# Kernel tuning notes

Measured on AMD Instinct MI355X. Metric: run time of the kernel, lower is better.

Reference implementation:

```python
import jax, jax.numpy as jnp
import numpy as np

N_HEADS = 8
EPS = 1e-5  # torch nn.LayerNorm default


def layer_norm(x, g, b):
    mu = jnp.mean(x, axis=-1, keepdims=True)
    var = jnp.var(x, axis=-1, keepdims=True)
    return (x - mu) * jax.lax.rsqrt(var + EPS) * g + b


def mha(q_in, k_in, v_in, adj, Wq, bq, Wk, bk, Wv, bv, Wo, bo, g, be):
    # Standard GL-GIN / Co-guiding MultiHeadAttention: proj -> adjacency-masked
    # scaled dot-product softmax -> out proj -> residual + LayerNorm.
    # Dropout omitted (eval mode).
    B, Lq, D = q_in.shape
    Lk = k_in.shape[1]
    d_k = Wq.shape[-1] // N_HEADS
    q = (q_in @ Wq + bq).reshape(B, Lq, N_HEADS, d_k)
    k = (k_in @ Wk + bk).reshape(B, Lk, N_HEADS, d_k)
    v = (v_in @ Wv + bv).reshape(B, Lk, N_HEADS, d_k)
    scale = jnp.asarray(1.0 / np.sqrt(d_k), q_in.dtype)
    scores = jnp.einsum('bqhd,bkhd->bhqk', q, k) * scale  # [B,H,Lq,Lk]
    neg = jnp.asarray(-1e9, scores.dtype)
    scores = jnp.where(adj[:, None, :, :] == 0, neg, scores)
    attn = jax.nn.softmax(scores, axis=-1)
    out = jnp.einsum('bhqk,bkhd->bqhd', attn, v).reshape(B, Lq, N_HEADS * d_k)
    out = out @ Wo + bo
    return layer_norm(out + q_in, g, be)


def co_guiding_forward(h_a, h_b, adj_a, adj_b, adj_ab, adj_ba,
                       Wq, bq, Wk, bk, Wv, bv, Wo, bo, ln_g, ln_b):
    # Param arrays are stacked [n_layer, 4, ...], branch order: a2a, b2b, a2b, b2a.
    input_a, input_b = h_a, h_b
    n_layer = Wq.shape[0]
    for i in range(n_layer):
        def P(j):
            return (Wq[i, j], bq[i, j], Wk[i, j], bk[i, j], Wv[i, j], bv[i, j],
                    Wo[i, j], bo[i, j], ln_g[i, j], ln_b[i, j])
        a2a = mha(h_a, h_a, h_a, adj_a, *P(0))
        b2b = mha(h_b, h_b, h_b, adj_b, *P(1))
        a2b = mha(h_b, h_a, h_a, adj_ab, *P(2))
        b2a = mha(h_a, h_b, h_b, adj_ba, *P(3))
        h_a = jax.nn.relu(a2a + b2a)
        h_b = jax.nn.relu(b2b + a2b)
    return input_a + h_a, input_b + h_b


def setup_inputs():
    key = jax.random.key(0)
    ks = jax.random.split(key, 16)
    B, N, D, L = 4, 1024, 256, 2
    f = lambda k, s: jax.random.normal(k, s, dtype=jnp.float32) * 0.05
    return {
        'h_a': jax.random.normal(ks[0], (B, N, D), dtype=jnp.float32),
        'h_b': jax.random.normal(ks[1], (B, N, D), dtype=jnp.float32),
        'adj_a': jax.random.randint(ks[2], (B, N, N), 0, 2, dtype=jnp.int32),
        'adj_b': jax.random.randint(ks[3], (B, N, N), 0, 2, dtype=jnp.int32),
        'adj_ab': jax.random.randint(ks[4], (B, N, N), 0, 2, dtype=jnp.int32),
        'adj_ba': jax.random.randint(ks[5], (B, N, N), 0, 2, dtype=jnp.int32),
        'Wq': f(ks[6], (L, 4, D, D)), 'bq': f(ks[7], (L, 4, D)),
        'Wk': f(ks[8], (L, 4, D, D)), 'bk': f(ks[9], (L, 4, D)),
        'Wv': f(ks[10], (L, 4, D, D)), 'bv': f(ks[11], (L, 4, D)),
        'Wo': f(ks[12], (L, 4, D, D)), 'bo': f(ks[13], (L, 4, D)),
        'ln_g': jnp.ones((L, 4, D), dtype=jnp.float32),
        'ln_b': jnp.zeros((L, 4, D), dtype=jnp.float32),
    }


def reference(h_a, h_b, adj_a, adj_b, adj_ab, adj_ba,
              Wq, bq, Wk, bk, Wv, bv, Wo, bo, ln_g, ln_b):
    return co_guiding_forward(h_a, h_b, adj_a, adj_b, adj_ab, adj_ba,
                              Wq, bq, Wk, bk, Wv, bv, Wo, bo, ln_g, ln_b)
```

## Files before the change

kernel.cpp:

```cpp
#include <hip/hip_runtime.h>
#include <hip/hip_bf16.h>
#include <stdint.h>


using bf16x8 = __attribute__((ext_vector_type(8))) short;
using f32x4  = __attribute__((ext_vector_type(4))) float;
using f32x16 = __attribute__((ext_vector_type(16))) float;

#define DEVI __device__ __forceinline__

DEVI uint16_t f2bf(float x) {
  uint32_t u = __float_as_uint(x);
  u += 0x7FFFu + ((u >> 16) & 1u);
  return (uint16_t)(u >> 16);
}
DEVI uint32_t packbf2(float lo, float hi) {
  uint32_t r;
  asm("v_cvt_pk_bf16_f32 %0, %1, %2" : "=v"(r) : "v"(lo), "v"(hi));
  return r;
}
DEVI float bf2f(uint16_t v) { return __uint_as_float((uint32_t)v << 16); }
DEVI int phi4(int m) {
  return ((m & 4) << 1) | ((m & 8) >> 1) | (m & 3);
}

struct PrepArgs {
  const float* Wq; const float* Wk; const float* Wv; const float* Wo;
  uint16_t* wt;
  const float* ha; const float* hb;
  uint16_t* oa; uint16_t* ob;
  const int* adj[4];
  uint32_t* bits[4];
};

__global__ __launch_bounds__(256) void prep_k(PrepArgs a) {
  const int blk = blockIdx.x;
  const int t = threadIdx.x;
  __shared__ float tl[64][68];

  if (blk < 512) {
    const int bx = blk & 3, by = (blk >> 2) & 3, z = blk >> 4;
    const int type = z >> 3, mat = z & 7;
    const float* W = (type == 0 ? a.Wq : type == 1 ? a.Wk : type == 2 ? a.Wv : a.Wo)
                     + (size_t)mat * 65536;
    uint16_t* o = a.wt + (size_t)type * 524288 + (size_t)mat * 65536;
    const int r0 = by * 64, c0 = bx * 64;
    {
      const int rr = t >> 2, cb = (t & 3) * 16;
      const float* src = W + (size_t)(r0 + rr) * 256 + c0 + cb;
      #pragma unroll
      for (int q = 0; q < 4; ++q) {
        float4 v = *(const float4*)(src + q * 4);
        tl[rr][cb + q*4 + 0] = v.x; tl[rr][cb + q*4 + 1] = v.y;
        tl[rr][cb + q*4 + 2] = v.z; tl[rr][cb + q*4 + 3] = v.w;
      }
    }
    __syncthreads();
    {
      const int nn = t >> 2, kb = (t & 3) * 16;
      __align__(16) uint16_t tmp[16];
      #pragma unroll
      for (int q = 0; q < 16; ++q) tmp[q] = f2bf(tl[kb + q][nn]);
      uint16_t* dst = o + (size_t)(c0 + nn) * 256 + r0 + kb;
      *(uint4*)&dst[0] = *(uint4*)&tmp[0];
      *(uint4*)&dst[8] = *(uint4*)&tmp[8];
    }
  } else if (blk < 1536) {
    const int idx = blk - 512;
    const int bx = idx & 511, by = idx >> 9;
    const size_t i = ((size_t)bx * 256 + t) * 8;
    const float* s = by ? a.hb : a.ha;
    uint16_t* o = by ? a.ob : a.oa;
    const float4 f0 = *(const float4*)(s + i), f1 = *(const float4*)(s + i + 4);
    uint4 u;
    u.x = packbf2(f0.x, f0.y); u.y = packbf2(f0.z, f0.w);
    u.z = packbf2(f1.x, f1.y); u.w = packbf2(f1.z, f1.w);
    *(uint4*)(o + i) = u;
  } else {
    const int idx = blk - 1536;
    const int bx = idx & 16383, z = idx >> 14;
    const int* adj = a.adj[z];
    uint32_t* bits = a.bits[z];
    const size_t i = (size_t)bx * 256 + t;
    const int lane = t & 63;
    const int v = adj[i];
    unsigned long long m = __ballot(v != 0);
    if ((lane & 31) == 0) {
      const uint32_t wi = (uint32_t)(i >> 5);
      const uint32_t kw = wi & 31;
      const uint32_t q  = (wi >> 5) & 1023;
      const uint32_t bb = wi >> 15;
      bits[((bb * 32 + kw) << 10) | q] = (uint32_t)(m >> (lane & 32));
    }
  }
}

struct GemmArgs {
  const uint16_t* A[12];
  const uint16_t* W[12];
  const float*    bias[12];
  void*           C[12];
  float           os[12];
  int             mode[12];
};

DEVI void stage_tile(const uint16_t* __restrict__ Ab,
                     const uint16_t* __restrict__ Wt,
                     int m0, int n0, int kk,
                     char* AsB, char* BsB, int wid, int lane) {
  #pragma unroll
  for (int i = 0; i < 2; ++i) {
    const int seg = i * 4 + wid;
    const int rl  = (seg << 4) + (lane >> 2);
    const int gs  = (lane & 3) ^ ((lane >> 3) & 3);
    const uint16_t* gA = Ab + (size_t)(m0 + rl) * 256 + kk + gs * 8;
    const uint16_t* gB = Wt + (size_t)(n0 + rl) * 256 + kk + gs * 8;
    __builtin_amdgcn_global_load_lds(
        (const __attribute__((address_space(1))) void*)gA,
        (__attribute__((address_space(3))) void*)(AsB + (seg << 10)), 16, 0, 0);
    __builtin_amdgcn_global_load_lds(
        (const __attribute__((address_space(1))) void*)gB,
        (__attribute__((address_space(3))) void*)(BsB + (seg << 10)), 16, 0, 0);
  }
}

__global__ __launch_bounds__(256) void gemm_k(GemmArgs args) {
  const int z  = blockIdx.z;
  const int m0 = blockIdx.y * 128, n0 = blockIdx.x * 128;
  const uint16_t* Ab = args.A[z];
  const uint16_t* Wt = args.W[z];
  __shared__ __align__(16) uint16_t As[2][4096];
  __shared__ __align__(16) uint16_t Bs[2][4096];
  const int t = threadIdx.x;
  const int lane = t & 63, wid = t >> 6;
  const int g = lane >> 4, c = lane & 15;
  const int gx = g ^ ((c >> 1) & 3);
  const int wm = (wid >> 1) * 64, wn = (wid & 1) * 64;
  f32x4 acc[4][4] = {};

  stage_tile(Ab, Wt, m0, n0, 0, (char*)As[0], (char*)Bs[0], wid, lane);
  __syncthreads();

  for (int ks = 0; ks < 8; ++ks) {
    const int buf = ks & 1;
    if (ks < 7)
      stage_tile(Ab, Wt, m0, n0, (ks + 1) * 32,
                 (char*)As[buf ^ 1], (char*)Bs[buf ^ 1], wid, lane);
    bf16x8 af[4], bfr[4];
    #pragma unroll
    for (int mt = 0; mt < 4; ++mt)
      af[mt]  = *(const bf16x8*)&As[buf][(wm + mt * 16 + c) * 32 + gx * 8];
    #pragma unroll
    for (int nt = 0; nt < 4; ++nt)
      bfr[nt] = *(const bf16x8*)&Bs[buf][(wn + nt * 16 + c) * 32 + gx * 8];
    #pragma unroll
    for (int mt = 0; mt < 4; ++mt)
      #pragma unroll
      for (int nt = 0; nt < 4; ++nt)
        acc[mt][nt] = __builtin_amdgcn_mfma_f32_16x16x32_bf16(af[mt], bfr[nt], acc[mt][nt], 0, 0, 0);
    if (ks < 7) __syncthreads();
  }

  const float* bias = args.bias[z];
  const float osz = args.os[z];
  const int mode = args.mode[z];
  float bv[4];
  #pragma unroll
  for (int nt = 0; nt < 4; ++nt) bv[nt] = bias[n0 + wn + nt * 16 + c];

  if (mode == 2) {
    uint16_t* C = (uint16_t*)args.C[z];
    __syncthreads();
    uint16_t* ep = ((uint16_t*)As) + wid * (16 * 72);
    #pragma unroll
    for (int mt = 0; mt < 4; ++mt) {
      #pragma unroll
      for (int r = 0; r < 4; ++r)
        #pragma unroll
        for (int nt = 0; nt < 4; ++nt)
          ep[(4 * g + r) * 72 + nt * 16 + c] = f2bf((acc[mt][nt][r] + bv[nt]) * osz);
      #pragma unroll
      for (int sr = 0; sr < 2; ++sr) {
        const int row  = sr * 8 + (lane >> 3);
        const int col8 = (lane & 7) * 8;
        const uint4 v4 = *(const uint4*)&ep[row * 72 + col8];
        const int n  = m0 + wm + mt * 16 + row;
        const int bb = n >> 10, nn = n & 1023;
        const int colg = n0 + wn + col8;
        const int hh = colg >> 5, d = colg & 31;
        *(uint4*)&C[((size_t)(bb * 8 + hh) * 1024 + nn) * 32 + d] = v4;
      }
    }
  } else {
    uint16_t* C = (uint16_t*)args.C[z];
    __syncthreads();
    uint16_t* ep = ((uint16_t*)As) + wid * (64 * 24);
    const int colg = n0 + wn + lane;
    const int hh = colg >> 5, d = colg & 31;
    #pragma unroll
    for (int mt = 0; mt < 4; ++mt) {
      #pragma unroll
      for (int r = 0; r < 4; ++r) {
        const int pn = phi4(4 * g + r);
        #pragma unroll
        for (int nt = 0; nt < 4; ++nt)
          ep[(nt * 16 + c) * 24 + pn] = f2bf((acc[mt][nt][r] + bv[nt]) * osz);
      }
      const int nbase = m0 + wm + mt * 16;
      const int bb = nbase >> 10, nb = nbase & 1023;
      uint16_t* dst = C + ((size_t)(bb * 8 + hh) * 32 + d) * 1024 + nb;
      *(uint4*)dst       = *(const uint4*)&ep[lane * 24];
      *(uint4*)(dst + 8) = *(const uint4*)&ep[lane * 24 + 8];
    }
  }
}

struct AttnArgs {
  const uint16_t* Q[4];
  const uint16_t* K[4];
  const uint16_t* Vt[4];
  const uint32_t* adjb[4];
  uint16_t*       O[4];
};

DEVI void soft_pv(f32x16& st, uint32_t w, float& l,
                  const bf16x8& vf0, const bf16x8& vf1, f32x16& oacc) {
  float s0 = 0.f, s1 = 0.f, s2 = 0.f, s3 = 0.f;
  #pragma unroll
  for (int r = 0; r < 16; ++r) {
    const int pos = (r & 3) + 8 * (r >> 2);
    const uint32_t msk = (uint32_t)__builtin_amdgcn_sbfe((int)w, pos, 1);
    const float pv = __uint_as_float(
        __float_as_uint(__builtin_amdgcn_exp2f(st[r])) & msk);
    st[r] = pv;
    if ((r & 3) == 0) s0 += pv; else if ((r & 3) == 1) s1 += pv;
    else if ((r & 3) == 2) s2 += pv; else s3 += pv;
  }
  l += (s0 + s1) + (s2 + s3);

  union PU { uint32_t u[4]; bf16x8 v; };
  PU p0, p1;
  p0.u[0] = packbf2(st[0],  st[1]);  p0.u[1] = packbf2(st[2],  st[3]);
  p0.u[2] = packbf2(st[4],  st[5]);  p0.u[3] = packbf2(st[6],  st[7]);
  p1.u[0] = packbf2(st[8],  st[9]);  p1.u[1] = packbf2(st[10], st[11]);
  p1.u[2] = packbf2(st[12], st[13]); p1.u[3] = packbf2(st[14], st[15]);

  oacc = __builtin_amdgcn_mfma_f32_32x32x16_bf16(vf0, p0.v, oacc, 0, 0, 0);
  oacc = __builtin_amdgcn_mfma_f32_32x32x16_bf16(vf1, p1.v, oacc, 0, 0, 0);
}

__global__ __launch_bounds__(256) void attn_k(AttnArgs args) {
  const int bid = blockIdx.x;
  const int qt  = bid >> 7;
  const int grp = bid & 127;
  const int bh = grp & 31, j = grp >> 5;
  const int b = bh >> 3, h = bh & 7;
  const int t = threadIdx.x, wid = t >> 6, lane = t & 63;
  const int qg = wid & 1, ks = wid >> 1;
  const int c = lane & 31, hi = lane >> 5;
  const int hsh = hi * 4;
  const int qrow = qt * 128 + qg * 64 + c;

  const uint16_t* Qbh = args.Q[j] + (size_t)(b * 8 + h) * 32768;
  const uint16_t* Kbh = args.K[j] + (size_t)(b * 8 + h) * 32768;
  const uint16_t* Vbh = args.Vt[j] + ((size_t)(b * 8 + h) * 32 + c) * 1024 + hi * 8;

  const bf16x8 qa0 = *(const bf16x8*)&Qbh[qrow * 32 + hi * 8];
  const bf16x8 qa1 = *(const bf16x8*)&Qbh[qrow * 32 + 16 + hi * 8];
  const bf16x8 qb0 = *(const bf16x8*)&Qbh[(qrow + 32) * 32 + hi * 8];
  const bf16x8 qb1 = *(const bf16x8*)&Qbh[(qrow + 32) * 32 + 16 + hi * 8];

  f32x16 oA = {}, oB = {};
  float lA = 0.f, lB = 0.f;

  const int kbeg = ks * 512;
  const uint16_t* kp = Kbh + (size_t)(kbeg + c) * 32 + hi * 8;
  const uint16_t* vp = Vbh + kbeg;
  const uint32_t* ap = args.adjb[j] + (size_t)b * 32768
                       + ((size_t)(kbeg >> 5) << 10) + qrow;

  for (int it = 0; it < 16; ++it) {
    const uint32_t wA = ap[0]  >> hsh;
    const uint32_t wB = ap[32] >> hsh;
    const bf16x8 kf0 = *(const bf16x8*)kp;
    const bf16x8 kf1 = *(const bf16x8*)(kp + 16);
    const bf16x8 vf0 = *(const bf16x8*)vp;
    const bf16x8 vf1 = *(const bf16x8*)(vp + 16);
    ap += 1024; kp += 1024; vp += 32;

    f32x16 sA = {}, sB = {};
    sA = __builtin_amdgcn_mfma_f32_32x32x16_bf16(kf0, qa0, sA, 0, 0, 0);
    sA = __builtin_amdgcn_mfma_f32_32x32x16_bf16(kf1, qa1, sA, 0, 0, 0);
    sB = __builtin_amdgcn_mfma_f32_32x32x16_bf16(kf0, qb0, sB, 0, 0, 0);
    sB = __builtin_amdgcn_mfma_f32_32x32x16_bf16(kf1, qb1, sB, 0, 0, 0);

    soft_pv(sA, wA, lA, vf0, vf1, oA);
    soft_pv(sB, wB, lB, vf0, vf1, oB);
  }

  __shared__ float red[2][2][64][17];
  if (ks == 1) {
    #pragma unroll
    for (int r = 0; r < 16; ++r) {
      red[qg][0][lane][r] = oA[r];
      red[qg][1][lane][r] = oB[r];
    }
    red[qg][0][lane][16] = lA;
    red[qg][1][lane][16] = lB;
  }
  __syncthreads();
  if (ks == 1) return;

  {
    #pragma unroll
    for (int r = 0; r < 16; ++r) {
      oA[r] += red[qg][0][lane][r];
      oB[r] += red[qg][1][lane][r];
    }
    lA += red[qg][0][lane][16];
    lB += red[qg][1][lane][16];
  }

  lA += __shfl_xor(lA, 32, 64);
  lB += __shfl_xor(lB, 32, 64);
  const float invA = 1.0f / lA;
  const float invB = 1.0f / lB;
  uint16_t* O = args.O[j];
  const size_t obA = (size_t)(b * 1024 + qrow) * 256 + h * 32 + 4 * hi;
  const size_t obB = obA + (size_t)32 * 256;
  #pragma unroll
  for (int rq = 0; rq < 4; ++rq) {
    uint2 vA, vB;
    vA.x = packbf2(oA[4*rq+0] * invA, oA[4*rq+1] * invA);
    vA.y = packbf2(oA[4*rq+2] * invA, oA[4*rq+3] * invA);
    vB.x = packbf2(oB[4*rq+0] * invB, oB[4*rq+1] * invB);
    vB.y = packbf2(oB[4*rq+2] * invB, oB[4*rq+3] * invB);
    *(uint2*)&O[obA + 8 * rq] = vA;
    *(uint2*)&O[obB + 8 * rq] = vB;
  }
}

struct OplnArgs {
  const uint16_t* A0[2]; const uint16_t* A1[2];
  const uint16_t* W0[2]; const uint16_t* W1[2];
  const float*    b0[2]; const float*    b1[2];
  const uint16_t* res[2];
  const float* g0[2]; const float* be0[2];
  const float* g1[2]; const float* be1[2];
  const float* addin[2];
  float*     outf[2];
  uint16_t*  outbf[2];
};

__global__ __launch_bounds__(256) void opln_k(OplnArgs args) {
  const int side = blockIdx.y;
  const int m0 = blockIdx.x * 32;
  const uint16_t* A0 = args.A0[side];
  const uint16_t* A1 = args.A1[side];
  const uint16_t* W0 = args.W0[side];
  const uint16_t* W1 = args.W1[side];

  __shared__ __align__(16) char lds[76800];
  uint16_t* As0 = (uint16_t*)(lds);
  uint16_t* As1 = (uint16_t*)(lds + 4096);
  uint16_t* Bs0 = (uint16_t*)(lds + 8192);
  uint16_t* Bs1 = (uint16_t*)(lds + 8192 + 32768);
  float*    red = (float*)(lds + 8192 + 65536);
  float*    muv = (float*)(lds + 8192 + 65536 + 2048);
  uint16_t* outt = (uint16_t*)lds;

  const int t = threadIdx.x;
  const int lane = t & 63, wid = t >> 6;
  const int g = lane >> 4, c = lane & 15;
  const int gx = g ^ ((c >> 1) & 3);
  const int gs = (lane & 3) ^ ((lane >> 3) & 3);

  auto stage = [&](int buf, int kk) {
    {
      const uint16_t* src = (wid < 2) ? A0 : A1;
      char* dst = (char*)((wid < 2) ? As0 : As1) + (size_t)buf * 2048 + ((wid & 1) << 10);
      const int rl = ((wid & 1) << 4) + (lane >> 2);
      __builtin_amdgcn_global_load_lds(
          (const __attribute__((address_space(1))) void*)(src + (size_t)(m0 + rl) * 256 + kk + gs * 8),
          (__attribute__((address_space(3))) void*)dst, 16, 0, 0);
    }
    #pragma unroll
    for (int i = 0; i < 8; ++i) {
      const int s32 = i * 4 + wid;
      const int mat = s32 >> 4, seg = s32 & 15;
      const uint16_t* src = mat ? W1 : W0;
      char* dst = (char*)(mat ? Bs1 : Bs0) + (size_t)buf * 16384 + (seg << 10);
      const int rl = (seg << 4) + (lane >> 2);
      __builtin_amdgcn_global_load_lds(
          (const __attribute__((address_space(1))) void*)(src + (size_t)rl * 256 + kk + gs * 8),
          (__attribute__((address_space(3))) void*)dst, 16, 0, 0);
    }
  };

  f32x4 a0[2][4] = {}, a1[2][4] = {};
  stage(0, 0);
  __syncthreads();

  for (int ks = 0; ks < 8; ++ks) {
    const int buf = ks & 1;
    if (ks < 7) stage(buf ^ 1, (ks + 1) * 32);
    const uint16_t* As0b = As0 + buf * 1024;
    const uint16_t* As1b = As1 + buf * 1024;
    const uint16_t* Bs0b = Bs0 + buf * 8192;
    const uint16_t* Bs1b = Bs1 + buf * 8192;
    bf16x8 fa0[2], fa1[2], fb0[4], fb1[4];
    #pragma unroll
    for (int mt = 0; mt < 2; ++mt) {
      fa0[mt] = *(const bf16x8*)&As0b[(mt * 16 + c) * 32 + gx * 8];
      fa1[mt] = *(const bf16x8*)&As1b[(mt * 16 + c) * 32 + gx * 8];
    }
    #pragma unroll
    for (int nt = 0; nt < 4; ++nt) {
      fb0[nt] = *(const bf16x8*)&Bs0b[(wid * 64 + nt * 16 + c) * 32 + gx * 8];
      fb1[nt] = *(const bf16x8*)&Bs1b[(wid * 64 + nt * 16 + c) * 32 + gx * 8];
    }
    #pragma unroll
    for (int mt = 0; mt < 2; ++mt)
      #pragma unroll
      for (int nt = 0; nt < 4; ++nt) {
        a0[mt][nt] = __builtin_amdgcn_mfma_f32_16x16x32_bf16(fa0[mt], fb0[nt], a0[mt][nt], 0, 0, 0);
        a1[mt][nt] = __builtin_amdgcn_mfma_f32_16x16x32_bf16(fa1[mt], fb1[nt], a1[mt][nt], 0, 0, 0);
      }
    if (ks < 7) __syncthreads();
  }

  const float* b0p = args.b0[side];
  const float* b1p = args.b1[side];
  const uint16_t* resp = args.res[side];
  float bv0[4], bv1[4];
  #pragma unroll
  for (int nt = 0; nt < 4; ++nt) {
    bv0[nt] = b0p[wid * 64 + nt * 16 + c];
    bv1[nt] = b1p[wid * 64 + nt * 16 + c];
  }
  #pragma unroll
  for (int mt = 0; mt < 2; ++mt)
    #pragma unroll
    for (int r = 0; r < 4; ++r) {
      const int row = mt * 16 + 4 * g + r;
      #pragma unroll
      for (int nt = 0; nt < 4; ++nt) {
        const float rf = bf2f(resp[(size_t)(m0 + row) * 256 + wid * 64 + nt * 16 + c]);
        a0[mt][nt][r] = a0[mt][nt][r] + bv0[nt] + rf;
        a1[mt][nt][r] = a1[mt][nt][r] + bv1[nt] + rf;
      }
    }

  #pragma unroll
  for (int mt = 0; mt < 2; ++mt)
    #pragma unroll
    for (int r = 0; r < 4; ++r) {
      float s0 = 0.f, ss0 = 0.f, s1 = 0.f, ss1 = 0.f;
      #pragma unroll
      for (int nt = 0; nt < 4; ++nt) {
        const float x0 = a0[mt][nt][r], x1 = a1[mt][nt][r];
        s0 += x0; ss0 += x0 * x0; s1 += x1; ss1 += x1 * x1;
      }
      #pragma unroll
      for (int m = 1; m < 16; m <<= 1) {
        s0 += __shfl_xor(s0, m, 64);  ss0 += __shfl_xor(ss0, m, 64);
        s1 += __shfl_xor(s1, m, 64);  ss1 += __shfl_xor(ss1, m, 64);
      }
      if (c == 0) {
        const int row = mt * 16 + 4 * g + r;
        float* rp = red + (row * 4 + wid) * 4;
        rp[0] = s0; rp[1] = ss0; rp[2] = s1; rp[3] = ss1;
      }
    }
  __syncthreads();

  if (t < 32) {
    float S0 = 0.f, SS0 = 0.f, S1 = 0.f, SS1 = 0.f;
    #pragma unroll
    for (int w = 0; w < 4; ++w) {
      const float* rp = red + (t * 4 + w) * 4;
      S0 += rp[0]; SS0 += rp[1]; S1 += rp[2]; SS1 += rp[3];
    }
    const float mu0 = S0 * (1.f / 256.f);
    const float mu1 = S1 * (1.f / 256.f);
    const float rs0 = rsqrtf(SS0 * (1.f / 256.f) - mu0 * mu0 + 1e-5f);
    const float rs1 = rsqrtf(SS1 * (1.f / 256.f) - mu1 * mu1 + 1e-5f);
    float* mp = muv + t * 4;
    mp[0] = mu0; mp[1] = rs0; mp[2] = mu1; mp[3] = rs1;
  }
  __syncthreads();

  const float* g0p = args.g0[side];  const float* be0p = args.be0[side];
  const float* g1p = args.g1[side];  const float* be1p = args.be1[side];
  float ga0[4], bb0[4], ga1[4], bb1[4];
  #pragma unroll
  for (int nt = 0; nt < 4; ++nt) {
    const int col = wid * 64 + nt * 16 + c;
    ga0[nt] = g0p[col]; bb0[nt] = be0p[col];
    ga1[nt] = g1p[col]; bb1[nt] = be1p[col];
  }
  #pragma unroll
  for (int mt = 0; mt < 2; ++mt)
    #pragma unroll
    for (int r = 0; r < 4; ++r) {
      const int row = mt * 16 + 4 * g + r;
      const float4 m4 = *(const float4*)(muv + row * 4);
      #pragma unroll
      for (int nt = 0; nt < 4; ++nt) {
        const float y = fmaxf((a0[mt][nt][r] - m4.x) * m4.y * ga0[nt] + bb0[nt]
                            + (a1[mt][nt][r] - m4.z) * m4.w * ga1[nt] + bb1[nt], 0.f);
        outt[row * 272 + wid * 64 + nt * 16 + c] = f2bf(y);
      }
    }
  __syncthreads();

  const int orow = t >> 3, ocb = (t & 7) * 32;
  if (args.addin[side]) {
    const float* ad = args.addin[side] + (size_t)(m0 + orow) * 256 + ocb;
    float* of = args.outf[side] + (size_t)(m0 + orow) * 256 + ocb;
    #pragma unroll
    for (int q = 0; q < 8; ++q) {
      const float4 av = *(const float4*)(ad + q * 4);
      float4 y4;
      y4.x = bf2f(outt[orow * 272 + ocb + q * 4 + 0]) + av.x;
      y4.y = bf2f(outt[orow * 272 + ocb + q * 4 + 1]) + av.y;
      y4.z = bf2f(outt[orow * 272 + ocb + q * 4 + 2]) + av.z;
      y4.w = bf2f(outt[orow * 272 + ocb + q * 4 + 3]) + av.w;
      *(float4*)(of + q * 4) = y4;
    }
  } else {
    uint16_t* ob = args.outbf[side] + (size_t)(m0 + orow) * 256 + ocb;
    #pragma unroll
    for (int q = 0; q < 4; ++q)
      *(uint4*)(ob + q * 8) = *(const uint4*)&outt[orow * 272 + ocb + q * 8];
  }
}

extern "C" void kernel_launch(void* const* d_in, const int* in_sizes, int n_in,
                              void* d_out, int out_size, void* d_ws, size_t ws_size,
                              hipStream_t stream) {
  (void)in_sizes; (void)n_in; (void)out_size; (void)ws_size;
  const float* h_a = (const float*)d_in[0];
  const float* h_b = (const float*)d_in[1];
  const float* bq  = (const float*)d_in[7];
  const float* bk  = (const float*)d_in[9];
  const float* bv  = (const float*)d_in[11];
  const float* bo  = (const float*)d_in[13];
  const float* lng = (const float*)d_in[14];
  const float* lnb = (const float*)d_in[15];

  const float QSC = 1.4426950408889634f * 0.17677669529663687f;

  char* ws = (char*)d_ws;
  uint16_t* WT   = (uint16_t*)ws;
  uint32_t* ADJB = (uint32_t*)(ws + (4u  << 20));
  uint16_t* hAbf = (uint16_t*)(ws + (6u  << 20));
  uint16_t* hBbf = (uint16_t*)(ws + (8u  << 20));
  uint16_t* Qb[4]; uint16_t* Kb[4]; uint16_t* Vtb[4]; uint16_t* ATb[4];
  for (int j = 0; j < 4; ++j) {
    Qb[j]  = (uint16_t*)(ws + (10u << 20) + (size_t)j * (2u << 20));
    Kb[j]  = (uint16_t*)(ws + (18u << 20) + (size_t)j * (2u << 20));
    Vtb[j] = (uint16_t*)(ws + (26u << 20) + (size_t)j * (2u << 20));
    ATb[j] = (uint16_t*)(ws + (34u << 20) + (size_t)j * (2u << 20));
  }

  {
    PrepArgs pa;
    pa.Wq = (const float*)d_in[6];  pa.Wk = (const float*)d_in[8];
    pa.Wv = (const float*)d_in[10]; pa.Wo = (const float*)d_in[12];
    pa.wt = WT;
    pa.ha = h_a; pa.hb = h_b; pa.oa = hAbf; pa.ob = hBbf;
    for (int j = 0; j < 4; ++j) {
      pa.adj[j]  = (const int*)d_in[2 + j];
      pa.bits[j] = ADJB + (size_t)j * 131072;
    }
    prep_k<<<dim3(67072, 1, 1), 256, 0, stream>>>(pa);
  }

  for (int i = 0; i < 2; ++i) {
    const uint16_t* qbf[4]  = { hAbf, hBbf, hBbf, hAbf };
    const uint16_t* kvbf[4] = { hAbf, hBbf, hAbf, hBbf };

    {
      GemmArgs ga = {};
      for (int j = 0; j < 4; ++j) {
        const int mm = i * 4 + j;
        ga.A[j]     = qbf[j];  ga.W[j]     = WT + 0 * 524288 + (size_t)mm * 65536;
        ga.bias[j]  = bq + mm * 256; ga.C[j] = Qb[j];  ga.os[j] = QSC;  ga.mode[j] = 2;
        ga.A[4+j]   = kvbf[j]; ga.W[4+j]   = WT + 1 * 524288 + (size_t)mm * 65536;
        ga.bias[4+j]= bk + mm * 256; ga.C[4+j] = Kb[j]; ga.os[4+j] = 1.0f; ga.mode[4+j] = 2;
        ga.A[8+j]   = kvbf[j]; ga.W[8+j]   = WT + 2 * 524288 + (size_t)mm * 65536;
        ga.bias[8+j]= bv + mm * 256; ga.C[8+j] = Vtb[j]; ga.os[8+j] = 1.0f; ga.mode[8+j] = 3;
      }
      gemm_k<<<dim3(2, 32, 12), 256, 0, stream>>>(ga);
    }
    {
      AttnArgs at;
      for (int j = 0; j < 4; ++j) {
        at.Q[j] = Qb[j]; at.K[j] = Kb[j]; at.Vt[j] = Vtb[j];
        at.adjb[j] = ADJB + (size_t)j * 131072; at.O[j] = ATb[j];
      }
      attn_k<<<dim3(1024, 1, 1), 256, 0, stream>>>(at);
    }
    {
      OplnArgs oa;
      const int j0[2] = {0, 1}, j1[2] = {3, 2};
      for (int s = 0; s < 2; ++s) {
        const int mm0 = i * 4 + j0[s], mm1 = i * 4 + j1[s];
        oa.A0[s] = ATb[j0[s]];  oa.A1[s] = ATb[j1[s]];
        oa.W0[s] = WT + 3 * 524288 + (size_t)mm0 * 65536;
        oa.W1[s] = WT + 3 * 524288 + (size_t)mm1 * 65536;
        oa.b0[s] = bo + mm0 * 256;  oa.b1[s] = bo + mm1 * 256;
        oa.res[s] = s ? hBbf : hAbf;
        oa.g0[s] = lng + mm0 * 256;  oa.be0[s] = lnb + mm0 * 256;
        oa.g1[s] = lng + mm1 * 256;  oa.be1[s] = lnb + mm1 * 256;
        if (i == 1) {
          oa.addin[s] = s ? h_b : h_a;
          oa.outf[s]  = (float*)d_out + (size_t)s * 1048576;
          oa.outbf[s] = nullptr;
        } else {
          oa.addin[s] = nullptr;
          oa.outf[s]  = nullptr;
          oa.outbf[s] = s ? hBbf : hAbf;
        }
      }
      opln_k<<<dim3(128, 2), 256, 0, stream>>>(oa);
    }
  }
}
```

Measured before the change: 189.9 us.

## Load weight fragments directly from global memory and add MFMA priority hints

The GEMM and fused output-projection/LayerNorm kernels no longer stage the weight (B) tiles through LDS. Each wave now reads its bf16 weight fragments straight from global memory into registers, which cuts LDS use in opln_k sharply and should allow more resident blocks. The attention kernel wraps its MFMA groups in s_setprio to favour matrix issue, and the bf16 pack switches from inline asm to the HIP intrinsic. The risk is that weight reads now depend on cache hits and global latency that sits inside the inner loop instead of being hidden by the double buffer.

```diff
diff --git a/kernel.cpp b/kernel.cpp
--- a/kernel.cpp
+++ b/kernel.cpp
@@ -15,9 +15,9 @@
   return (uint16_t)(u >> 16);
 }
 DEVI uint32_t packbf2(float lo, float hi) {
-  uint32_t r;
-  asm("v_cvt_pk_bf16_f32 %0, %1, %2" : "=v"(r) : "v"(lo), "v"(hi));
-  return r;
+  union { __hip_bfloat162 h; uint32_t u; } cv;
+  cv.h = __float22bfloat162_rn(make_float2(lo, hi));
+  return cv.u;
 }
 DEVI float bf2f(uint16_t v) { return __uint_as_float((uint32_t)v << 16); }
 DEVI int phi4(int m) {
@@ -104,23 +104,17 @@
   int             mode[12];
 };
 
-DEVI void stage_tile(const uint16_t* __restrict__ Ab,
-                     const uint16_t* __restrict__ Wt,
-                     int m0, int n0, int kk,
-                     char* AsB, char* BsB, int wid, int lane) {
+DEVI void stage_A(const uint16_t* __restrict__ Ab, int m0, int kk,
+                  char* AsB, int wid, int lane) {
   #pragma unroll
   for (int i = 0; i < 2; ++i) {
     const int seg = i * 4 + wid;
     const int rl  = (seg << 4) + (lane >> 2);
     const int gs  = (lane & 3) ^ ((lane >> 3) & 3);
     const uint16_t* gA = Ab + (size_t)(m0 + rl) * 256 + kk + gs * 8;
-    const uint16_t* gB = Wt + (size_t)(n0 + rl) * 256 + kk + gs * 8;
     __builtin_amdgcn_global_load_lds(
         (const __attribute__((address_space(1))) void*)gA,
         (__attribute__((address_space(3))) void*)(AsB + (seg << 10)), 16, 0, 0);
-    __builtin_amdgcn_global_load_lds(
-        (const __attribute__((address_space(1))) void*)gB,
-        (__attribute__((address_space(3))) void*)(BsB + (seg << 10)), 16, 0, 0);
   }
 }
 
@@ -130,7 +124,6 @@
   const uint16_t* Ab = args.A[z];
   const uint16_t* Wt = args.W[z];
   __shared__ __align__(16) uint16_t As[2][4096];
-  __shared__ __align__(16) uint16_t Bs[2][4096];
   const int t = threadIdx.x;
   const int lane = t & 63, wid = t >> 6;
   const int g = lane >> 4, c = lane & 15;
@@ -138,21 +131,25 @@
   const int wm = (wid >> 1) * 64, wn = (wid & 1) * 64;
   f32x4 acc[4][4] = {};
 
-  stage_tile(Ab, Wt, m0, n0, 0, (char*)As[0], (char*)Bs[0], wid, lane);
+  const uint16_t* bp[4];
+  #pragma unroll
+  for (int nt = 0; nt < 4; ++nt)
+    bp[nt] = Wt + (size_t)(n0 + wn + nt * 16 + c) * 256 + g * 8;
+
+  stage_A(Ab, m0, 0, (char*)As[0], wid, lane);
   __syncthreads();
 
   for (int ks = 0; ks < 8; ++ks) {
     const int buf = ks & 1;
     if (ks < 7)
-      stage_tile(Ab, Wt, m0, n0, (ks + 1) * 32,
-                 (char*)As[buf ^ 1], (char*)Bs[buf ^ 1], wid, lane);
+      stage_A(Ab, m0, (ks + 1) * 32, (char*)As[buf ^ 1], wid, lane);
     bf16x8 af[4], bfr[4];
+    #pragma unroll
+    for (int nt = 0; nt < 4; ++nt)
+      bfr[nt] = *(const bf16x8*)(bp[nt] + ks * 32);
     #pragma unroll
     for (int mt = 0; mt < 4; ++mt)
       af[mt]  = *(const bf16x8*)&As[buf][(wm + mt * 16 + c) * 32 + gx * 8];
-    #pragma unroll
-    for (int nt = 0; nt < 4; ++nt)
-      bfr[nt] = *(const bf16x8*)&Bs[buf][(wn + nt * 16 + c) * 32 + gx * 8];
     #pragma unroll
     for (int mt = 0; mt < 4; ++mt)
       #pragma unroll
@@ -245,8 +242,10 @@
   p1.u[0] = packbf2(st[8],  st[9]);  p1.u[1] = packbf2(st[10], st[11]);
   p1.u[2] = packbf2(st[12], st[13]); p1.u[3] = packbf2(st[14], st[15]);
 
+  __builtin_amdgcn_s_setprio(1);
   oacc = __builtin_amdgcn_mfma_f32_32x32x16_bf16(vf0, p0.v, oacc, 0, 0, 0);
   oacc = __builtin_amdgcn_mfma_f32_32x32x16_bf16(vf1, p1.v, oacc, 0, 0, 0);
+  __builtin_amdgcn_s_setprio(0);
 }
 
 __global__ __launch_bounds__(256) void attn_k(AttnArgs args) {
@@ -289,10 +288,12 @@
     ap += 1024; kp += 1024; vp += 32;
 
     f32x16 sA = {}, sB = {};
+    __builtin_amdgcn_s_setprio(1);
     sA = __builtin_amdgcn_mfma_f32_32x32x16_bf16(kf0, qa0, sA, 0, 0, 0);
     sA = __builtin_amdgcn_mfma_f32_32x32x16_bf16(kf1, qa1, sA, 0, 0, 0);
     sB = __builtin_amdgcn_mfma_f32_32x32x16_bf16(kf0, qb0, sB, 0, 0, 0);
     sB = __builtin_amdgcn_mfma_f32_32x32x16_bf16(kf1, qb1, sB, 0, 0, 0);
+    __builtin_amdgcn_s_setprio(0);
 
     soft_pv(sA, wA, lA, vf0, vf1, oA);
     soft_pv(sB, wB, lB, vf0, vf1, oB);
@@ -360,14 +361,12 @@
   const uint16_t* W0 = args.W0[side];
   const uint16_t* W1 = args.W1[side];
 
-  __shared__ __align__(16) char lds[76800];
+  __shared__ __align__(16) char lds[20480];
   uint16_t* As0 = (uint16_t*)(lds);
   uint16_t* As1 = (uint16_t*)(lds + 4096);
-  uint16_t* Bs0 = (uint16_t*)(lds + 8192);
-  uint16_t* Bs1 = (uint16_t*)(lds + 8192 + 32768);
-  float*    red = (float*)(lds + 8192 + 65536);
-  float*    muv = (float*)(lds + 8192 + 65536 + 2048);
   uint16_t* outt = (uint16_t*)lds;
+  float*    red = (float*)(lds + 17664);
+  float*    muv = (float*)(lds + 19712);
 
   const int t = threadIdx.x;
   const int lane = t & 63, wid = t >> 6;
@@ -375,49 +374,42 @@
   const int gx = g ^ ((c >> 1) & 3);
   const int gs = (lane & 3) ^ ((lane >> 3) & 3);
 
-  auto stage = [&](int buf, int kk) {
-    {
-      const uint16_t* src = (wid < 2) ? A0 : A1;
-      char* dst = (char*)((wid < 2) ? As0 : As1) + (size_t)buf * 2048 + ((wid & 1) << 10);
-      const int rl = ((wid & 1) << 4) + (lane >> 2);
-      __builtin_amdgcn_global_load_lds(
-          (const __attribute__((address_space(1))) void*)(src + (size_t)(m0 + rl) * 256 + kk + gs * 8),
-          (__attribute__((address_space(3))) void*)dst, 16, 0, 0);
-    }
-    #pragma unroll
-    for (int i = 0; i < 8; ++i) {
-      const int s32 = i * 4 + wid;
-      const int mat = s32 >> 4, seg = s32 & 15;
-      const uint16_t* src = mat ? W1 : W0;
-      char* dst = (char*)(mat ? Bs1 : Bs0) + (size_t)buf * 16384 + (seg << 10);
-      const int rl = (seg << 4) + (lane >> 2);
-      __builtin_amdgcn_global_load_lds(
-          (const __attribute__((address_space(1))) void*)(src + (size_t)rl * 256 + kk + gs * 8),
-          (__attribute__((address_space(3))) void*)dst, 16, 0, 0);
-    }
+  auto stageA = [&](int buf, int kk) {
+    const uint16_t* src = (wid < 2) ? A0 : A1;
+    char* dst = (char*)((wid < 2) ? As0 : As1) + (size_t)buf * 2048 + ((wid & 1) << 10);
+    const int rl = ((wid & 1) << 4) + (lane >> 2);
+    __builtin_amdgcn_global_load_lds(
+        (const __attribute__((address_space(1))) void*)(src + (size_t)(m0 + rl) * 256 + kk + gs * 8),
+        (__attribute__((address_space(3))) void*)dst, 16, 0, 0);
   };
 
+  const uint16_t* bp0[4];
+  const uint16_t* bp1[4];
+  #pragma unroll
+  for (int nt = 0; nt < 4; ++nt) {
+    bp0[nt] = W0 + (size_t)(wid * 64 + nt * 16 + c) * 256 + g * 8;
+    bp1[nt] = W1 + (size_t)(wid * 64 + nt * 16 + c) * 256 + g * 8;
+  }
+
   f32x4 a0[2][4] = {}, a1[2][4] = {};
-  stage(0, 0);
+  stageA(0, 0);
   __syncthreads();
 
   for (int ks = 0; ks < 8; ++ks) {
     const int buf = ks & 1;
-    if (ks < 7) stage(buf ^ 1, (ks + 1) * 32);
+    if (ks < 7) stageA(buf ^ 1, (ks + 1) * 32);
     const uint16_t* As0b = As0 + buf * 1024;
     const uint16_t* As1b = As1 + buf * 1024;
-    const uint16_t* Bs0b = Bs0 + buf * 8192;
-    const uint16_t* Bs1b = Bs1 + buf * 8192;
     bf16x8 fa0[2], fa1[2], fb0[4], fb1[4];
+    #pragma unroll
+    for (int nt = 0; nt < 4; ++nt) {
+      fb0[nt] = *(const bf16x8*)(bp0[nt] + ks * 32);
+      fb1[nt] = *(const bf16x8*)(bp1[nt] + ks * 32);
+    }
     #pragma unroll
     for (int mt = 0; mt < 2; ++mt) {
       fa0[mt] = *(const bf16x8*)&As0b[(mt * 16 + c) * 32 + gx * 8];
       fa1[mt] = *(const bf16x8*)&As1b[(mt * 16 + c) * 32 + gx * 8];
-    }
-    #pragma unroll
-    for (int nt = 0; nt < 4; ++nt) {
-      fb0[nt] = *(const bf16x8*)&Bs0b[(wid * 64 + nt * 16 + c) * 32 + gx * 8];
-      fb1[nt] = *(const bf16x8*)&Bs1b[(wid * 64 + nt * 16 + c) * 32 + gx * 8];
     }
     #pragma unroll
     for (int mt = 0; mt < 2; ++mt)
```

Result: slower. 205.5 us (+8.2%).
